# Optimization experiments

Hardware: AMD Instinct MI355X
Metric: run time of the kernel (lower is better)

The kernel has to match this reference:

```python
import jax, jax.numpy as jnp
import numpy as np

N_USER = 50000
N_ITEM = 100000
N_NODES = N_USER + N_ITEM  # 150000
EMB = 64
N_LAYERS = 3
NNZ = 2400000
BATCH = 4096
EPS = 1e-12  # F.normalize eps


def setup_inputs() -> dict:
    key = jax.random.key(0)
    ks = jax.random.split(key, 12)
    return {
        "users": jax.random.randint(ks[0], (BATCH,), 0, N_USER, dtype=jnp.int32),
        "pos_items": jax.random.randint(ks[1], (BATCH,), 0, N_ITEM, dtype=jnp.int32),
        "neg_items": jax.random.randint(ks[2], (BATCH,), 0, N_ITEM, dtype=jnp.int32),
        "adj_row": jax.random.randint(ks[3], (NNZ,), 0, N_NODES, dtype=jnp.int32),
        "adj_col": jax.random.randint(ks[4], (NNZ,), 0, N_NODES, dtype=jnp.int32),
        "adj_val": jax.random.uniform(ks[5], (NNZ,), dtype=jnp.float32),
        "user_emb": jax.random.normal(ks[6], (N_USER, EMB), dtype=jnp.float32) * 0.1,
        "item_emb": jax.random.normal(ks[7], (N_ITEM, EMB), dtype=jnp.float32) * 0.1,
        "W_gc": jax.random.normal(ks[8], (N_LAYERS, EMB, EMB), dtype=jnp.float32) * 0.1,
        "b_gc": jax.random.normal(ks[9], (N_LAYERS, 1, EMB), dtype=jnp.float32) * 0.1,
        "W_bi": jax.random.normal(ks[10], (N_LAYERS, EMB, EMB), dtype=jnp.float32) * 0.1,
        "b_bi": jax.random.normal(ks[11], (N_LAYERS, 1, EMB), dtype=jnp.float32) * 0.1,
    }


def reference(users, pos_items, neg_items, adj_row, adj_col, adj_val,
              user_emb, item_emb, W_gc, b_gc, W_bi, b_bi):
    # ego embeddings: concat user/item tables -> [N_NODES, EMB]
    ego = jnp.concatenate([user_emb, item_emb], axis=0)
    all_embs = [ego]
    for k in range(N_LAYERS):
        # sparse A_hat @ ego via gather + segment-sum over edges
        msgs = adj_val[:, None] * ego[adj_col]            # [NNZ, EMB]
        side = jax.ops.segment_sum(msgs, adj_row, num_segments=N_NODES)
        sum_emb = side @ W_gc[k] + b_gc[k]                # [N, EMB]
        bi_emb = (ego * side) @ W_bi[k] + b_bi[k]         # [N, EMB]
        ego = jax.nn.leaky_relu(sum_emb + bi_emb, negative_slope=0.2)
        # mess_dropout = 0 (eval mode) -> identity
        nrm = jnp.linalg.norm(ego, axis=1, keepdims=True)
        all_embs.append(ego / jnp.maximum(nrm, EPS))
    all_embs = jnp.concatenate(all_embs, axis=1)          # [N, EMB*(L+1)]
    u_g = all_embs[:N_USER]
    i_g = all_embs[N_USER:]
    return (u_g[users], i_g[pos_items], i_g[neg_items])
```

## Files before the change

kernel.cpp:

```cpp
#include <hip/hip_runtime.h>

typedef short bf16x8 __attribute__((ext_vector_type(8)));
typedef float f32x4  __attribute__((ext_vector_type(4)));

#define N_USER 50000
#define N_ITEM 100000
#define N_NODES 150000
#define EMB 64
#define NNZ 2400000
#define BATCH 4096
#define NSAMP (3 * BATCH)
#define NB 512
#define RPB 293
#define BS_GRID 500
#define EPB (NNZ / BS_GRID)
#define CAP 5312

__device__ __forceinline__ unsigned int bf16_rne(float x) {
    unsigned int u = __float_as_uint(x);
    return (u + 0x7fffu + ((u >> 16) & 1u)) >> 16;
}
__device__ __forceinline__ float bflo(unsigned int u) { return __uint_as_float(u << 16); }
__device__ __forceinline__ float bfhi(unsigned int u) { return __uint_as_float(u & 0xffff0000u); }

__device__ __forceinline__ void fma8(float v, const uint4& x, float* acc) {
    acc[0] = fmaf(v, bflo(x.x), acc[0]); acc[1] = fmaf(v, bfhi(x.x), acc[1]);
    acc[2] = fmaf(v, bflo(x.y), acc[2]); acc[3] = fmaf(v, bfhi(x.y), acc[3]);
    acc[4] = fmaf(v, bflo(x.z), acc[4]); acc[5] = fmaf(v, bfhi(x.z), acc[5]);
    acc[6] = fmaf(v, bflo(x.w), acc[6]); acc[7] = fmaf(v, bfhi(x.w), acc[7]);
}
__device__ __forceinline__ uint4 pack8(const float* f) {
    return make_uint4((bf16_rne(f[1]) << 16) | bf16_rne(f[0]),
                      (bf16_rne(f[3]) << 16) | bf16_rne(f[2]),
                      (bf16_rne(f[5]) << 16) | bf16_rne(f[4]),
                      (bf16_rne(f[7]) << 16) | bf16_rne(f[6]));
}
__device__ __forceinline__ uint2 cvt2(const float4& v) {
    return make_uint2((bf16_rne(v.y) << 16) | bf16_rne(v.x),
                      (bf16_rne(v.w) << 16) | bf16_rne(v.z));
}

#define SEG_A (N_NODES * 4)
#define SEG_B (NSAMP * 16)
#define SEG_C (3 * 8192)
#define SEG_D 192
#define INIT_TOT (SEG_A + SEG_B + SEG_C + SEG_D + NSAMP)
#define INIT_BLOCKS ((INIT_TOT + 1023) / 1024)
__global__ __launch_bounds__(1024) void scat_init(const int* __restrict__ rows,
                                                  const int* __restrict__ cols,
                                                  const float* __restrict__ vals,
                                                  int* __restrict__ gcur,
                                                  int2* __restrict__ tmp_cv,
                                                  const float4* __restrict__ ue4,
                                                  const float4* __restrict__ ie4,
                                                  const int* __restrict__ users,
                                                  const int* __restrict__ pos,
                                                  const int* __restrict__ neg,
                                                  uint2* __restrict__ ego_bf,
                                                  float* __restrict__ out,
                                                  int* __restrict__ samp,
                                                  const float* __restrict__ Wgc,
                                                  const float* __restrict__ Wbi,
                                                  const float* __restrict__ bgc,
                                                  const float* __restrict__ bbi,
                                                  ushort* __restrict__ wbf,
                                                  float* __restrict__ biasf) {
    __shared__ int2 sorted[EPB];
    __shared__ int hist[NB];
    __shared__ int excl[NB];
    __shared__ int cur[NB];
    __shared__ int gb[NB];
    const int t = threadIdx.x;
    if (blockIdx.x < BS_GRID) {
        const int blk = blockIdx.x;
        if (t < NB) { hist[t] = 0; cur[t] = 0; }
        __syncthreads();
        const int e0 = blk * EPB;
        for (int i = t; i < EPB; i += 1024) atomicAdd(&hist[rows[e0 + i] / RPB], 1);
        __syncthreads();
        if (t < NB) gb[t] = atomicAdd(&gcur[t], hist[t]);
        if (t < NB) excl[t] = hist[t];
        for (int off = 1; off < NB; off <<= 1) {
            __syncthreads();
            int add = (t < NB && t >= off) ? excl[t - off] : 0;
            __syncthreads();
            if (t < NB) excl[t] += add;
        }
        __syncthreads();
        for (int i = t; i < EPB; i += 1024) {
            int e = e0 + i;
            int r = rows[e];
            int b = r / RPB;
            int slot = atomicAdd(&cur[b], 1);
            unsigned vv = (__float_as_uint(vals[e]) & ~1023u) | (unsigned)(r - b * RPB);
            sorted[excl[b] - hist[b] + slot] = make_int2(cols[e], (int)vv);
        }
        __syncthreads();
        const int w = t >> 6, lane = t & 63;
        for (int b = w; b < NB; b += 16) {
            int lo = excl[b] - hist[b];
            int n = hist[b];
            int2* dst = tmp_cv + (size_t)b * CAP + gb[b];
            for (int k = lane; k < n; k += 64) dst[k] = sorted[lo + k];
        }
        return;
    }
    int idx = (blockIdx.x - BS_GRID) * 1024 + t;
    if (idx >= INIT_TOT) return;
    if (idx < SEG_A) {
        const int NU4 = N_USER * 16;
        int b4 = idx * 4;
        float4 a, b, c, d;
        if (b4 < NU4) { a = ue4[b4]; b = ue4[b4 + 1]; c = ue4[b4 + 2]; d = ue4[b4 + 3]; }
        else { int j = b4 - NU4; a = ie4[j]; b = ie4[j + 1]; c = ie4[j + 2]; d = ie4[j + 3]; }
        uint2 o0 = cvt2(a), o1 = cvt2(b), o2 = cvt2(c), o3 = cvt2(d);
        uint4* e4 = (uint4*)ego_bf;
        e4[idx * 2]     = make_uint4(o0.x, o0.y, o1.x, o1.y);
        e4[idx * 2 + 1] = make_uint4(o2.x, o2.y, o3.x, o3.y);
    } else if (idx < SEG_A + SEG_B) {
        int tt = idx - SEG_A;
        int r = tt >> 4, dq = tt & 15;
        int seg = r >> 12, bi = r & (BATCH - 1);
        int node = (seg == 0) ? users[bi] : N_USER + ((seg == 1) ? pos[bi] : neg[bi]);
        float4 v = (node < N_USER) ? ue4[node * 16 + dq] : ie4[(node - N_USER) * 16 + dq];
        ((float4*)out)[(size_t)r * 64 + dq] = v;
    } else if (idx < SEG_A + SEG_B + SEG_C) {
        int tt = idx - SEG_A - SEG_B;
        int l = tt >> 13, rem = tt & 8191;
        int k = rem >> 6, n = rem & 63;
        float w = (k < 64) ? Wgc[l * 4096 + k * 64 + n] : Wbi[l * 4096 + (k - 64) * 64 + n];
        wbf[l * 8704 + n * 136 + k] = (ushort)bf16_rne(w);
    } else if (idx < SEG_A + SEG_B + SEG_C + SEG_D) {
        int tt = idx - SEG_A - SEG_B - SEG_C;
        biasf[tt] = bgc[tt] + bbi[tt];
    } else {
        int tt = idx - SEG_A - SEG_B - SEG_C - SEG_D;
        int seg = tt >> 12, bi = tt & (BATCH - 1);
        samp[tt] = (seg == 0) ? users[bi] : N_USER + ((seg == 1) ? pos[bi] : neg[bi]);
    }
}

__global__ __launch_bounds__(1024) void csr_from_bins(const int* __restrict__ gcur,
                                                      const int2* __restrict__ tmp_cv,
                                                      int2* __restrict__ ecv,
                                                      int2* __restrict__ row_se) {
    __shared__ int2 stage[CAP];
    __shared__ int rcur[RPB];
    __shared__ int sc[1024];
    const int b = blockIdx.x;
    const int row0 = b * RPB;
    const int t = threadIdx.x;
    const int beg = b * CAP;
    const int cnt = gcur[b];

    if (t < RPB) rcur[t] = 0;
    __syncthreads();
    for (int i = t; i < cnt; i += 1024) {
        int2 rec = tmp_cv[beg + i];
        stage[i] = rec;
        atomicAdd(&rcur[rec.y & 1023], 1);
    }
    __syncthreads();

    int v = (t < RPB) ? rcur[t] : 0;
    sc[t] = v;
    for (int off = 1; off < 1024; off <<= 1) {
        __syncthreads();
        int add = (t >= off) ? sc[t - off] : 0;
        __syncthreads();
        sc[t] += add;
    }
    __syncthreads();
    int ex = sc[t] - v;

    int lim = N_NODES - row0;
    if (lim > RPB) lim = RPB;
    if (t < lim) row_se[row0 + t] = make_int2(beg + ex, beg + ex + v);
    if (t < RPB) rcur[t] = ex;
    __syncthreads();
    for (int i = t; i < cnt; i += 1024) {
        int2 rec = stage[i];
        int r10 = rec.y & 1023;
        int dst = beg + atomicAdd(&rcur[r10], 1);
        ecv[dst] = make_int2(rec.x, rec.y & ~1023);
    }
}

__global__ __launch_bounds__(256) void spmm_gemm(const int2* __restrict__ row_se,
                                                 const int2* __restrict__ ecv,
                                                 const uint4* __restrict__ ego_bf,
                                                 const ushort* __restrict__ wbf,
                                                 const float* __restrict__ biasf,
                                                 ushort* __restrict__ ego_out,
                                                 float* __restrict__ inv_norm,
                                                 float* __restrict__ out,
                                                 const int* __restrict__ node_list,
                                                 int n_rows, int out_mode, int col0,
                                                 const ushort* __restrict__ g_ego,
                                                 const float* __restrict__ g_inv,
                                                 const int* __restrict__ g_samp,
                                                 int g_col0) {
    const int t = threadIdx.x;
    const int spmmBlocks = (n_rows + 31) >> 5;
    if ((int)blockIdx.x >= spmmBlocks) {
        int i = (blockIdx.x - spmmBlocks) * 256 + t;
        int r = i >> 6, d = i & 63;
        int node = g_samp[r];
        float v = __uint_as_float(((unsigned int)g_ego[(size_t)node * 64 + d]) << 16) * g_inv[node];
        out[(size_t)r * 256 + g_col0 + d] = v;
        return;
    }

    __shared__ ushort As[32][136];

    const int d8 = t & 7;
    const int rl = t >> 3;
    const int r = blockIdx.x * 32 + rl;
    const bool valid = (r < n_rows);
    const int node = valid ? (node_list ? node_list[r] : r) : 0;
    int s0 = 0, s1 = 0;
    if (valid) { int2 se = row_se[node]; s0 = se.x; s1 = se.y; }
    const uint4 selfv = ego_bf[(size_t)node * 8 + d8];
    const int lbase = (t & 63) & 56;

    float acc[8] = {0.f, 0.f, 0.f, 0.f, 0.f, 0.f, 0.f, 0.f};
    int2 m = make_int2(0, 0);
    if (s0 + d8 < s1) m = ecv[s0 + d8];
    for (int e0 = s0; e0 < s1; e0 += 8) {
        int2 mn = make_int2(0, 0);
        if (e0 + 8 + d8 < s1) mn = ecv[e0 + 8 + d8];
#pragma unroll
        for (int j = 0; j < 8; ++j) {
            int   c = __shfl(m.x, lbase + j);
            float v = __int_as_float(__shfl(m.y, lbase + j));
            const uint4 x = ego_bf[(size_t)c * 8 + d8];
            fma8(v, x, acc);
        }
        m = mn;
    }
    float cs[8] = { bflo(selfv.x) * acc[0], bfhi(selfv.x) * acc[1],
                    bflo(selfv.y) * acc[2], bfhi(selfv.y) * acc[3],
                    bflo(selfv.z) * acc[4], bfhi(selfv.z) * acc[5],
                    bflo(selfv.w) * acc[6], bfhi(selfv.w) * acc[7] };
    *(uint4*)&As[rl][d8 * 8]      = pack8(acc);
    *(uint4*)&As[rl][64 + d8 * 8] = pack8(cs);
    __syncthreads();

    const int wv = t >> 6;
    if (wv >= 2) return;
    const int lane = t & 63;
    const int l15 = lane & 15, quad = lane >> 4;
    const bf16x8* wt8 = (const bf16x8*)wbf;
    const int arow = wv * 16 + l15;

    f32x4 C[4] = {{0,0,0,0}, {0,0,0,0}, {0,0,0,0}, {0,0,0,0}};
#pragma unroll
    for (int ks = 0; ks < 4; ++ks) {
        bf16x8 afr = *(const bf16x8*)&As[arow][(ks * 4 + quad) * 8];
        bf16x8 b0 = wt8[(0 * 16 + l15) * 17 + ks * 4 + quad];
        bf16x8 b1 = wt8[(1 * 16 + l15) * 17 + ks * 4 + quad];
        bf16x8 b2 = wt8[(2 * 16 + l15) * 17 + ks * 4 + quad];
        bf16x8 b3 = wt8[(3 * 16 + l15) * 17 + ks * 4 + quad];
        C[0] = __builtin_amdgcn_mfma_f32_16x16x32_bf16(afr, b0, C[0], 0, 0, 0);
        C[1] = __builtin_amdgcn_mfma_f32_16x16x32_bf16(afr, b1, C[1], 0, 0, 0);
        C[2] = __builtin_amdgcn_mfma_f32_16x16x32_bf16(afr, b2, C[2], 0, 0, 0);
        C[3] = __builtin_amdgcn_mfma_f32_16x16x32_bf16(afr, b3, C[3], 0, 0, 0);
    }

    float bias[4];
#pragma unroll
    for (int nt = 0; nt < 4; ++nt) bias[nt] = biasf[nt * 16 + l15];

    float x[4][4];
    float ss[4] = {0.f, 0.f, 0.f, 0.f};
#pragma unroll
    for (int nt = 0; nt < 4; ++nt)
#pragma unroll
        for (int rg = 0; rg < 4; ++rg) {
            float v = C[nt][rg] + bias[nt];
            v = (v >= 0.f) ? v : 0.2f * v;
            x[nt][rg] = v;
            ss[rg] = fmaf(v, v, ss[rg]);
        }
#pragma unroll
    for (int rg = 0; rg < 4; ++rg) {
        ss[rg] += __shfl_xor(ss[rg], 1);
        ss[rg] += __shfl_xor(ss[rg], 2);
        ss[rg] += __shfl_xor(ss[rg], 4);
        ss[rg] += __shfl_xor(ss[rg], 8);
    }
#pragma unroll
    for (int rg = 0; rg < 4; ++rg) {
        int row = blockIdx.x * 32 + wv * 16 + quad * 4 + rg;
        if (row >= n_rows) continue;
        float invr = 1.0f / fmaxf(sqrtf(ss[rg]), 1e-12f);
        if (out_mode) {
#pragma unroll
            for (int nt = 0; nt < 4; ++nt)
                out[(size_t)row * 256 + col0 + nt * 16 + l15] = x[nt][rg] * invr;
        } else {
#pragma unroll
            for (int nt = 0; nt < 4; ++nt)
                ego_out[(size_t)row * 64 + nt * 16 + l15] = (ushort)bf16_rne(x[nt][rg]);
            if (l15 == 0) inv_norm[row] = invr;
        }
    }
}

extern "C" void kernel_launch(void* const* d_in, const int* in_sizes, int n_in,
                              void* d_out, int out_size, void* d_ws, size_t ws_size,
                              hipStream_t stream) {
    const int* users = (const int*)d_in[0];
    const int* pos   = (const int*)d_in[1];
    const int* neg   = (const int*)d_in[2];
    const int* arow  = (const int*)d_in[3];
    const int* acol  = (const int*)d_in[4];
    const float* aval = (const float*)d_in[5];
    const float* ue   = (const float*)d_in[6];
    const float* ie   = (const float*)d_in[7];
    const float* Wgc  = (const float*)d_in[8];
    const float* bgc  = (const float*)d_in[9];
    const float* Wbi  = (const float*)d_in[10];
    const float* bbi  = (const float*)d_in[11];
    float* out = (float*)d_out;

    char* ws = (char*)d_ws;
    size_t o = 0;
    ushort* ego_a   = (ushort*)(ws + o); o += 19200000;
    ushort* ego_b   = (ushort*)(ws + o); o += 19200000;
    int2*   ecv     = (int2*)  (ws + o); o += (size_t)NB * CAP * 8;
    int2*   tmp_cv  = (int2*)  (ws + o); o += (size_t)NB * CAP * 8;
    int*    gcur    = (int*)   (ws + o); o += 2048;
    int2*   row_se  = (int2*)  (ws + o); o += 1200128;
    float*  inv_a     = (float*)(ws + o); o += 600064;
    float*  inv_b     = (float*)(ws + o); o += 600064;
    int*    samp      = (int*) (ws + o); o += 49152;
    ushort* wbf       = (ushort*)(ws + o); o += 52224;
    float*  biasf     = (float*)(ws + o); o += 768;

    const int gatherBlocks = (NSAMP * EMB) / 256;
    const int spmmN = (N_NODES + 31) / 32;
    const int spmmS = NSAMP / 32;

    hipMemsetAsync(gcur, 0, 2048, stream);
    scat_init<<<BS_GRID + INIT_BLOCKS, 1024, 0, stream>>>(
        arow, acol, aval, gcur, tmp_cv,
        (const float4*)ue, (const float4*)ie,
        users, pos, neg, (uint2*)ego_a, out, samp,
        Wgc, Wbi, bgc, bbi, wbf, biasf);
    csr_from_bins<<<NB, 1024, 0, stream>>>(gcur, tmp_cv, ecv, row_se);

    spmm_gemm<<<spmmN, 256, 0, stream>>>(
        row_se, ecv, (const uint4*)ego_a, wbf, biasf,
        ego_b, inv_b, out, nullptr, N_NODES, 0, 0,
        nullptr, nullptr, nullptr, 0);

    spmm_gemm<<<spmmN + gatherBlocks, 256, 0, stream>>>(
        row_se, ecv, (const uint4*)ego_b, wbf + 8704, biasf + 64,
        ego_a, inv_a, out, nullptr, N_NODES, 0, 0,
        ego_b, inv_b, samp, 64);

    spmm_gemm<<<spmmS + gatherBlocks, 256, 0, stream>>>(
        row_se, ecv, (const uint4*)ego_a, wbf + 2 * 8704, biasf + 128,
        nullptr, nullptr, out, samp, NSAMP, 1, 192,
        ego_a, inv_a, samp, 128);
}
```

Measured before the change: 290.7 us.

## Fuse CSR bin sort with first-layer SpMM and GEMM in one kernel

```diff
diff --git a/kernel.cpp b/kernel.cpp
--- a/kernel.cpp
+++ b/kernel.cpp
@@ -140,29 +140,37 @@
     }
 }
 
-__global__ __launch_bounds__(1024) void csr_from_bins(const int* __restrict__ gcur,
-                                                      const int2* __restrict__ tmp_cv,
-                                                      int2* __restrict__ ecv,
-                                                      int2* __restrict__ row_se) {
+__global__ __launch_bounds__(1024) void csr_spmm1(const int* __restrict__ gcur,
+                                                  const int2* __restrict__ tmp_cv,
+                                                  int2* __restrict__ ecv,
+                                                  int2* __restrict__ row_se,
+                                                  const uint4* __restrict__ ego_bf,
+                                                  const ushort* __restrict__ wbf,
+                                                  const float* __restrict__ biasf,
+                                                  ushort* __restrict__ ego_out,
+                                                  float* __restrict__ inv_norm) {
     __shared__ int2 stage[CAP];
-    __shared__ int rcur[RPB];
+    __shared__ int2 sorted2[CAP];
+    __shared__ ushort As3[4][32][136];
+    __shared__ int sstart[RPB + 1];
+    __shared__ int rcurs[RPB];
     __shared__ int sc[1024];
-    const int b = blockIdx.x;
+    const int b = blockIdx.x, t = threadIdx.x;
     const int row0 = b * RPB;
-    const int t = threadIdx.x;
     const int beg = b * CAP;
     const int cnt = gcur[b];
-
-    if (t < RPB) rcur[t] = 0;
+    int lim = N_NODES - row0;
+    if (lim > RPB) lim = RPB;
+
+    if (t < RPB) rcurs[t] = 0;
     __syncthreads();
     for (int i = t; i < cnt; i += 1024) {
         int2 rec = tmp_cv[beg + i];
         stage[i] = rec;
-        atomicAdd(&rcur[rec.y & 1023], 1);
-    }
-    __syncthreads();
-
-    int v = (t < RPB) ? rcur[t] : 0;
+        atomicAdd(&rcurs[rec.y & 1023], 1);
+    }
+    __syncthreads();
+    int v = (t < RPB) ? rcurs[t] : 0;
     sc[t] = v;
     for (int off = 1; off < 1024; off <<= 1) {
         __syncthreads();
@@ -172,17 +180,104 @@
     }
     __syncthreads();
     int ex = sc[t] - v;
-
-    int lim = N_NODES - row0;
-    if (lim > RPB) lim = RPB;
+    if (t <= RPB) sstart[t] = ex;
     if (t < lim) row_se[row0 + t] = make_int2(beg + ex, beg + ex + v);
-    if (t < RPB) rcur[t] = ex;
+    if (t < RPB) rcurs[t] = ex;
     __syncthreads();
     for (int i = t; i < cnt; i += 1024) {
         int2 rec = stage[i];
-        int r10 = rec.y & 1023;
-        int dst = beg + atomicAdd(&rcur[r10], 1);
-        ecv[dst] = make_int2(rec.x, rec.y & ~1023);
+        int dst = atomicAdd(&rcurs[rec.y & 1023], 1);
+        sorted2[dst] = make_int2(rec.x, rec.y & ~1023);
+    }
+    __syncthreads();
+    for (int i = t; i < cnt; i += 1024) ecv[beg + i] = sorted2[i];
+
+    const int w = t >> 6, lane = t & 63;
+    const int g = w >> 2, wig = w & 3;
+    const int d8 = lane & 7, rl = lane >> 3;
+    const int trow = wig * 8 + rl;
+    const int l15 = lane & 15, quad = lane >> 4;
+    const bf16x8* wt8 = (const bf16x8*)wbf;
+
+    for (int pass = 0; pass < 3; ++pass) {
+        int brow = pass * 128 + g * 32 + trow;
+        bool valid = (brow < lim);
+        int s0 = 0, s1 = 0;
+        if (valid) { s0 = sstart[brow]; s1 = sstart[brow + 1]; }
+        float acc[8] = {0.f, 0.f, 0.f, 0.f, 0.f, 0.f, 0.f, 0.f};
+        int j = s0;
+        for (; j + 4 <= s1; j += 4) {
+            int2 e0 = sorted2[j], e1 = sorted2[j + 1], e2 = sorted2[j + 2], e3 = sorted2[j + 3];
+            uint4 x0 = ego_bf[(size_t)e0.x * 8 + d8];
+            uint4 x1 = ego_bf[(size_t)e1.x * 8 + d8];
+            uint4 x2 = ego_bf[(size_t)e2.x * 8 + d8];
+            uint4 x3 = ego_bf[(size_t)e3.x * 8 + d8];
+            fma8(__int_as_float(e0.y), x0, acc);
+            fma8(__int_as_float(e1.y), x1, acc);
+            fma8(__int_as_float(e2.y), x2, acc);
+            fma8(__int_as_float(e3.y), x3, acc);
+        }
+        for (; j < s1; ++j) {
+            int2 e = sorted2[j];
+            uint4 x = ego_bf[(size_t)e.x * 8 + d8];
+            fma8(__int_as_float(e.y), x, acc);
+        }
+        int node = row0 + (valid ? brow : 0);
+        uint4 selfv = ego_bf[(size_t)node * 8 + d8];
+        float cs[8] = { bflo(selfv.x) * acc[0], bfhi(selfv.x) * acc[1],
+                        bflo(selfv.y) * acc[2], bfhi(selfv.y) * acc[3],
+                        bflo(selfv.z) * acc[4], bfhi(selfv.z) * acc[5],
+                        bflo(selfv.w) * acc[6], bfhi(selfv.w) * acc[7] };
+        *(uint4*)&As3[g][trow][d8 * 8]      = pack8(acc);
+        *(uint4*)&As3[g][trow][64 + d8 * 8] = pack8(cs);
+        __syncthreads();
+
+        if (wig < 2) {
+            const int arow = wig * 16 + l15;
+            f32x4 C[4] = {{0,0,0,0}, {0,0,0,0}, {0,0,0,0}, {0,0,0,0}};
+#pragma unroll
+            for (int ks = 0; ks < 4; ++ks) {
+                bf16x8 afr = *(const bf16x8*)&As3[g][arow][(ks * 4 + quad) * 8];
+                bf16x8 b0 = wt8[(0 * 16 + l15) * 17 + ks * 4 + quad];
+                bf16x8 b1 = wt8[(1 * 16 + l15) * 17 + ks * 4 + quad];
+                bf16x8 b2 = wt8[(2 * 16 + l15) * 17 + ks * 4 + quad];
+                bf16x8 b3 = wt8[(3 * 16 + l15) * 17 + ks * 4 + quad];
+                C[0] = __builtin_amdgcn_mfma_f32_16x16x32_bf16(afr, b0, C[0], 0, 0, 0);
+                C[1] = __builtin_amdgcn_mfma_f32_16x16x32_bf16(afr, b1, C[1], 0, 0, 0);
+                C[2] = __builtin_amdgcn_mfma_f32_16x16x32_bf16(afr, b2, C[2], 0, 0, 0);
+                C[3] = __builtin_amdgcn_mfma_f32_16x16x32_bf16(afr, b3, C[3], 0, 0, 0);
+            }
+            float x[4][4];
+            float ss[4] = {0.f, 0.f, 0.f, 0.f};
+#pragma unroll
+            for (int nt = 0; nt < 4; ++nt)
+#pragma unroll
+                for (int rg = 0; rg < 4; ++rg) {
+                    float vv = C[nt][rg] + biasf[nt * 16 + l15];
+                    vv = (vv >= 0.f) ? vv : 0.2f * vv;
+                    x[nt][rg] = vv;
+                    ss[rg] = fmaf(vv, vv, ss[rg]);
+                }
+#pragma unroll
+            for (int rg = 0; rg < 4; ++rg) {
+                ss[rg] += __shfl_xor(ss[rg], 1);
+                ss[rg] += __shfl_xor(ss[rg], 2);
+                ss[rg] += __shfl_xor(ss[rg], 4);
+                ss[rg] += __shfl_xor(ss[rg], 8);
+            }
+#pragma unroll
+            for (int rg = 0; rg < 4; ++rg) {
+                int bro = pass * 128 + g * 32 + wig * 16 + quad * 4 + rg;
+                if (bro >= lim) continue;
+                int grow = row0 + bro;
+                float invr = 1.0f / fmaxf(sqrtf(ss[rg]), 1e-12f);
+#pragma unroll
+                for (int nt = 0; nt < 4; ++nt)
+                    ego_out[(size_t)grow * 64 + nt * 16 + l15] = (ushort)bf16_rne(x[nt][rg]);
+                if (l15 == 0) inv_norm[grow] = invr;
+            }
+        }
+        __syncthreads();
     }
 }
 
@@ -348,12 +443,10 @@
         (const float4*)ue, (const float4*)ie,
         users, pos, neg, (uint2*)ego_a, out, samp,
         Wgc, Wbi, bgc, bbi, wbf, biasf);
-    csr_from_bins<<<NB, 1024, 0, stream>>>(gcur, tmp_cv, ecv, row_se);
-
-    spmm_gemm<<<spmmN, 256, 0, stream>>>(
-        row_se, ecv, (const uint4*)ego_a, wbf, biasf,
-        ego_b, inv_b, out, nullptr, N_NODES, 0, 0,
-        nullptr, nullptr, nullptr, 0);
+
+    csr_spmm1<<<NB, 1024, 0, stream>>>(
+        gcur, tmp_cv, ecv, row_se,
+        (const uint4*)ego_a, wbf, biasf, ego_b, inv_b);
 
     spmm_gemm<<<spmmN + gatherBlocks, 256, 0, stream>>>(
         row_se, ecv, (const uint4*)ego_b, wbf + 8704, biasf + 64,
```

After: 300.2 us. 3.3% more time.
